# Kernel tuning notes

Hardware: AMD Instinct MI355X
Metric: run time of the kernel (lower is better)

## Reference

```python
import jax, jax.numpy as jnp
import numpy as np
from jax import lax

TOL = 1e-06
POSINF = 1000000.0
NEGINF = -1000000.0


def _grad1(x, axis):
    """torch.gradient with spacing=1, edge_order=1 along `axis`:
    central differences in the interior, one-sided at the edges."""
    n = x.shape[axis]
    left = lax.slice_in_dim(x, 0, n - 2, axis=axis)
    right = lax.slice_in_dim(x, 2, n, axis=axis)
    interior = (right - left) * 0.5
    first = lax.slice_in_dim(x, 1, 2, axis=axis) - lax.slice_in_dim(x, 0, 1, axis=axis)
    last = lax.slice_in_dim(x, n - 1, n, axis=axis) - lax.slice_in_dim(x, n - 2, n - 1, axis=axis)
    return jnp.concatenate([first, interior, last], axis=axis)


def _clean(g):
    g = jnp.nan_to_num(g, nan=0.0, posinf=POSINF, neginf=NEGINF)
    return jnp.where(jnp.abs(g) < TOL, jnp.zeros_like(g), g)


def setup_inputs() -> dict:
    key = jax.random.key(0)
    k1, k2 = jax.random.split(key)
    shape = (8, 4, 64, 128, 128)  # [B, C=4, D, H, W]
    return {
        "input": jax.random.normal(k1, shape, dtype=jnp.float32),
        "target": jax.random.normal(k2, shape, dtype=jnp.float32),
    }


def reference(input, target):
    # spacing is ones per batch, so per-batch/per-channel loops collapse into
    # one vectorized finite-difference per spatial axis (dims 2, 3, 4).
    x = input.astype(jnp.float32)
    t = target.astype(jnp.float32)
    total = jnp.float32(0.0)
    for axis in (2, 3, 4):
        diff = _clean(_grad1(x, axis)) - _clean(_grad1(t, axis))
        # per-channel MSE (mean over b,d,h,w), then summed over the 4 channels
        total = total + jnp.sum(jnp.mean(diff * diff, axis=(0, 2, 3, 4)))
    return total
```

## Files before the change

kernel.cpp:

```cpp
#include <hip/hip_runtime.h>
#include <math.h>


#define Bn 8
#define Cn 4
#define Dn 64
#define Hn 128
#define Wn 128

static constexpr int HCHUNK = 8;
static constexpr int NTHREADS = 256;
static constexpr int NBLOCKS = 4096;
static constexpr int ROW = Wn / 4;
static constexpr int PLANE = Hn * ROW;

__device__ __forceinline__ float4 sub4(const float4 a, const float4 b) {
    float4 r;
    r.x = a.x - b.x; r.y = a.y - b.y;
    r.z = a.z - b.z; r.w = a.w - b.w;
    return r;
}

__global__ __launch_bounds__(NTHREADS, 4) void gradloss_main(
        const float* __restrict__ xf, const float* __restrict__ tf,
        double* __restrict__ partials) {
    const int tid  = threadIdx.x;
    const int w4   = tid & 31;
    const int dlow = tid >> 5;
    const int b    = blockIdx.x;
    const int bc    = b & 31;
    const int hc    = (b >> 5) & 15;
    const int dhigh = b >> 9;
    const int d  = dhigh * 8 + dlow;
    const int h0 = hc * HCHUNK;

    const int base = ((bc * Dn + d) * Hn + h0) * ROW + w4;
    const float4* __restrict__ Xr = (const float4*)xf + base;
    const float4* __restrict__ Tr = (const float4*)tf + base;

    const bool haloLow  = (dlow == 0);
    const bool haloHigh = (dlow == 7);
    const bool isHalo   = haloLow | haloHigh;
    const int hoff = haloLow ? ((dhigh > 0) ? -PLANE : 0)
                             : ((dhigh < 7) ?  PLANE : 0);

    const float sd2  = (d == 0 || d == Dn - 1) ? 1.0f : 0.25f;
    const float sw02 = (w4 == 0) ? 1.0f : 0.25f;
    const float sw32 = (w4 == 31) ? 1.0f : 0.25f;

    __shared__ float4 uL[2][10][32];

    float4 uc = sub4(Xr[0], Tr[0]);
    float4 um;
    if (h0 > 0) um = sub4(Xr[-ROW], Tr[-ROW]);
    else        um = uc;
    float4 hu;
    if (isHalo) hu = sub4(Xr[hoff], Tr[hoff]);
    else        hu = make_float4(0.f, 0.f, 0.f, 0.f);

    float acc0 = 0.0f, acc1 = 0.0f, acc2 = 0.0f;
    int s = 0;
    #pragma unroll
    for (int hl = 0; hl < HCHUNK; ++hl) {
        const int h = h0 + hl;
        const int po = (h < Hn - 1) ? ROW : 0;

        const float4 xn = Xr[po], tn = Tr[po];
        float4 xh, th;
        if (isHalo) { xh = Xr[hoff + po]; th = Tr[hoff + po]; }

        uL[s][dlow + 1][w4] = uc;
        if (haloLow)  uL[s][0][w4] = hu;
        if (haloHigh) uL[s][9][w4] = hu;
        __syncthreads();

        const float4 udp = uL[s][dlow + 2][w4];
        const float4 udm = uL[s][dlow][w4];
        { const float dx = udp.x - udm.x; acc1 = fmaf(dx * dx, sd2, acc1); }
        { const float dx = udp.y - udm.y; acc1 = fmaf(dx * dx, sd2, acc1); }
        { const float dx = udp.z - udm.z; acc1 = fmaf(dx * dx, sd2, acc1); }
        { const float dx = udp.w - udm.w; acc1 = fmaf(dx * dx, sd2, acc1); }

        const float ulw = __shfl_up(uc.w, 1, 32);
        const float urx = __shfl_down(uc.x, 1, 32);
        const float ul = (w4 == 0)  ? uc.x : ulw;
        const float ur = (w4 == 31) ? uc.w : urx;
        { const float dx = uc.y - ul;   acc2 = fmaf(dx * dx, sw02, acc2); }
        { const float dx = uc.z - uc.x; acc2 = fmaf(dx * dx, 0.25f, acc2); }
        { const float dx = uc.w - uc.y; acc2 = fmaf(dx * dx, 0.25f, acc2); }
        { const float dx = ur - uc.z;   acc2 = fmaf(dx * dx, sw32, acc2); }

        const float4 un = sub4(xn, tn);
        const float sh2 = (h == 0 || h == Hn - 1) ? 1.0f : 0.25f;
        { const float dx = un.x - um.x; acc0 = fmaf(dx * dx, sh2, acc0); }
        { const float dx = un.y - um.y; acc0 = fmaf(dx * dx, sh2, acc0); }
        { const float dx = un.z - um.z; acc0 = fmaf(dx * dx, sh2, acc0); }
        { const float dx = un.w - um.w; acc0 = fmaf(dx * dx, sh2, acc0); }

        um = uc; uc = un;
        if (isHalo) hu = sub4(xh, th);
        Xr += ROW; Tr += ROW;
        s ^= 1;
    }

    float acc = (acc0 + acc1) + acc2;

    for (int off = 32; off > 0; off >>= 1)
        acc += __shfl_down(acc, off, 64);

    __shared__ float wsum[NTHREADS / 64];
    const int lane = tid & 63;
    const int wid = tid >> 6;
    if (lane == 0) wsum[wid] = acc;
    __syncthreads();
    if (tid == 0) {
        double bsum = (double)wsum[0] + (double)wsum[1] +
                      (double)wsum[2] + (double)wsum[3];
        partials[blockIdx.x] = bsum;
    }
}

__global__ __launch_bounds__(256) void gradloss_reduce(
        const double* __restrict__ partials, float* __restrict__ out, int n) {
    double a = 0.0;
    for (int i = threadIdx.x; i < n; i += 256) a += partials[i];
    for (int off = 32; off > 0; off >>= 1)
        a += __shfl_down(a, off, 64);
    __shared__ double sh[4];
    const int lane = threadIdx.x & 63;
    const int wid = threadIdx.x >> 6;
    if (lane == 0) sh[wid] = a;
    __syncthreads();
    if (threadIdx.x == 0) {
        double tot = sh[0] + sh[1] + sh[2] + sh[3];
        out[0] = (float)(tot / 8388608.0);
    }
}

extern "C" void kernel_launch(void* const* d_in, const int* in_sizes, int n_in,
                              void* d_out, int out_size, void* d_ws, size_t ws_size,
                              hipStream_t stream) {
    const float* x = (const float*)d_in[0];
    const float* t = (const float*)d_in[1];
    float* out = (float*)d_out;
    double* partials = (double*)d_ws;

    gradloss_main<<<NBLOCKS, NTHREADS, 0, stream>>>(x, t, partials);
    gradloss_reduce<<<1, 256, 0, stream>>>(partials, out, NBLOCKS);
}
```

Baseline: 284.5 us.

## Replace LDS D-neighbor exchange with direct global loads and software prefetch

Drops the shared-memory staging and per-row __syncthreads used to exchange D-neighbor planes. Each thread now loads its own D+1 and D-1 values from global memory, relying on L2/cache hits, and double-buffers the next row's loads in registers. This removes barriers and LDS traffic, but roughly triples the global load instructions per thread and raises register pressure. The occupancy hint in launch_bounds is also dropped.

```diff
diff --git a/kernel.cpp b/kernel.cpp
--- a/kernel.cpp
+++ b/kernel.cpp
@@ -21,7 +21,21 @@
     return r;
 }
 
-__global__ __launch_bounds__(NTHREADS, 4) void gradloss_main(
+struct Step {
+    float4 xp, tp;
+    float4 xdp, tdp;
+    float4 xdm, tdm;
+};
+
+__device__ __forceinline__ void issue_step(
+        const float4* __restrict__ Xr, const float4* __restrict__ Tr,
+        int po, int dpo, int dmo, Step& s) {
+    s.xp  = Xr[po];  s.tp  = Tr[po];
+    s.xdp = Xr[dpo]; s.tdp = Tr[dpo];
+    s.xdm = Xr[dmo]; s.tdm = Tr[dmo];
+}
+
+__global__ __launch_bounds__(NTHREADS) void gradloss_main(
         const float* __restrict__ xf, const float* __restrict__ tf,
         double* __restrict__ partials) {
     const int tid  = threadIdx.x;
@@ -38,48 +52,38 @@
     const float4* __restrict__ Xr = (const float4*)xf + base;
     const float4* __restrict__ Tr = (const float4*)tf + base;
 
-    const bool haloLow  = (dlow == 0);
-    const bool haloHigh = (dlow == 7);
-    const bool isHalo   = haloLow | haloHigh;
-    const int hoff = haloLow ? ((dhigh > 0) ? -PLANE : 0)
-                             : ((dhigh < 7) ?  PLANE : 0);
-
+    const int dpo = (d < Dn - 1) ? PLANE : 0;
+    const int dmo = (d > 0) ? -PLANE : 0;
     const float sd2  = (d == 0 || d == Dn - 1) ? 1.0f : 0.25f;
     const float sw02 = (w4 == 0) ? 1.0f : 0.25f;
     const float sw32 = (w4 == 31) ? 1.0f : 0.25f;
 
-    __shared__ float4 uL[2][10][32];
-
-    float4 uc = sub4(Xr[0], Tr[0]);
-    float4 um;
-    if (h0 > 0) um = sub4(Xr[-ROW], Tr[-ROW]);
-    else        um = uc;
-    float4 hu;
-    if (isHalo) hu = sub4(Xr[hoff], Tr[hoff]);
-    else        hu = make_float4(0.f, 0.f, 0.f, 0.f);
+    const int mo = (h0 > 0) ? -ROW : 0;
+    const float4 xc0 = Xr[0],  tc0 = Tr[0];
+    const float4 xm0 = Xr[mo], tm0 = Tr[mo];
+    Step sbuf[2];
+    {
+        issue_step(Xr, Tr, ROW, dpo, dmo, sbuf[0]);
+    }
+    float4 uc = sub4(xc0, tc0);
+    float4 um = sub4(xm0, tm0);
 
     float acc0 = 0.0f, acc1 = 0.0f, acc2 = 0.0f;
-    int s = 0;
     #pragma unroll
     for (int hl = 0; hl < HCHUNK; ++hl) {
         const int h = h0 + hl;
-        const int po = (h < Hn - 1) ? ROW : 0;
 
-        const float4 xn = Xr[po], tn = Tr[po];
-        float4 xh, th;
-        if (isHalo) { xh = Xr[hoff + po]; th = Tr[hoff + po]; }
+        if (hl + 1 < HCHUNK) {
+            const int po2 = (h + 1 < Hn - 1) ? ROW : 0;
+            issue_step(Xr + ROW, Tr + ROW, po2, dpo, dmo, sbuf[(hl + 1) & 1]);
+        }
 
-        uL[s][dlow + 1][w4] = uc;
-        if (haloLow)  uL[s][0][w4] = hu;
-        if (haloHigh) uL[s][9][w4] = hu;
-        __syncthreads();
+        const Step& s = sbuf[hl & 1];
 
-        const float4 udp = uL[s][dlow + 2][w4];
-        const float4 udm = uL[s][dlow][w4];
-        { const float dx = udp.x - udm.x; acc1 = fmaf(dx * dx, sd2, acc1); }
-        { const float dx = udp.y - udm.y; acc1 = fmaf(dx * dx, sd2, acc1); }
-        { const float dx = udp.z - udm.z; acc1 = fmaf(dx * dx, sd2, acc1); }
-        { const float dx = udp.w - udm.w; acc1 = fmaf(dx * dx, sd2, acc1); }
+        { const float dx = (s.xdp.x - s.xdm.x) - (s.tdp.x - s.tdm.x); acc1 = fmaf(dx * dx, sd2, acc1); }
+        { const float dx = (s.xdp.y - s.xdm.y) - (s.tdp.y - s.tdm.y); acc1 = fmaf(dx * dx, sd2, acc1); }
+        { const float dx = (s.xdp.z - s.xdm.z) - (s.tdp.z - s.tdm.z); acc1 = fmaf(dx * dx, sd2, acc1); }
+        { const float dx = (s.xdp.w - s.xdm.w) - (s.tdp.w - s.tdm.w); acc1 = fmaf(dx * dx, sd2, acc1); }
 
         const float ulw = __shfl_up(uc.w, 1, 32);
         const float urx = __shfl_down(uc.x, 1, 32);
@@ -90,7 +94,7 @@
         { const float dx = uc.w - uc.y; acc2 = fmaf(dx * dx, 0.25f, acc2); }
         { const float dx = ur - uc.z;   acc2 = fmaf(dx * dx, sw32, acc2); }
 
-        const float4 un = sub4(xn, tn);
+        const float4 un = sub4(s.xp, s.tp);
         const float sh2 = (h == 0 || h == Hn - 1) ? 1.0f : 0.25f;
         { const float dx = un.x - um.x; acc0 = fmaf(dx * dx, sh2, acc0); }
         { const float dx = un.y - um.y; acc0 = fmaf(dx * dx, sh2, acc0); }
@@ -98,9 +102,7 @@
         { const float dx = un.w - um.w; acc0 = fmaf(dx * dx, sh2, acc0); }
 
         um = uc; uc = un;
-        if (isHalo) hu = sub4(xh, th);
         Xr += ROW; Tr += ROW;
-        s ^= 1;
     }
 
     float acc = (acc0 + acc1) + acc2;
```

New measurement: 290.5 us. 2.1% more time.

## Load whole H-chunk tile up front and drop per-row block barriers

Applied to the files above, without the earlier changes.

Each thread now issues all of its row loads (10 rows of x and t plus a cooperative load of the D-halo planes) at once into registers, writes the difference field into a 3D shared tile, and syncs once. The per-row double-buffered shared exchange with a __syncthreads each iteration is removed. This raises memory-level parallelism and removes the per-row barriers and divergent halo loads. In exchange it uses more registers and shared memory, and the occupancy hint of 4 blocks per SM is dropped.

```diff
diff --git a/kernel.cpp b/kernel.cpp
--- a/kernel.cpp
+++ b/kernel.cpp
@@ -8,7 +8,6 @@
 #define Hn 128
 #define Wn 128
 
-static constexpr int HCHUNK = 8;
 static constexpr int NTHREADS = 256;
 static constexpr int NBLOCKS = 4096;
 static constexpr int ROW = Wn / 4;
@@ -21,7 +20,7 @@
     return r;
 }
 
-__global__ __launch_bounds__(NTHREADS, 4) void gradloss_main(
+__global__ __launch_bounds__(NTHREADS) void gradloss_main(
         const float* __restrict__ xf, const float* __restrict__ tf,
         double* __restrict__ partials) {
     const int tid  = threadIdx.x;
@@ -30,57 +29,76 @@
     const int b    = blockIdx.x;
     const int bc    = b & 31;
     const int hc    = (b >> 5) & 15;
-    const int dhigh = b >> 9;
-    const int d  = dhigh * 8 + dlow;
-    const int h0 = hc * HCHUNK;
+    const int dt    = b >> 9;
+    const int d  = dt * 8 + dlow;
+    const int h0 = hc * 8;
 
-    const int base = ((bc * Dn + d) * Hn + h0) * ROW + w4;
-    const float4* __restrict__ Xr = (const float4*)xf + base;
-    const float4* __restrict__ Tr = (const float4*)tf + base;
+    const float4* __restrict__ X = (const float4*)xf;
+    const float4* __restrict__ T = (const float4*)tf;
+    const int slab  = bc * (Dn * PLANE);
+    const int pbase = slab + d * PLANE;
 
-    const bool haloLow  = (dlow == 0);
-    const bool haloHigh = (dlow == 7);
-    const bool isHalo   = haloLow | haloHigh;
-    const int hoff = haloLow ? ((dhigh > 0) ? -PLANE : 0)
-                             : ((dhigh < 7) ?  PLANE : 0);
+    float4 xr[10], tr[10];
+    #pragma unroll
+    for (int r = 0; r < 10; ++r) {
+        int h = h0 + r - 1;
+        h = (h < 0) ? 0 : ((h > Hn - 1) ? Hn - 1 : h);
+        const int idx = pbase + h * ROW + w4;
+        xr[r] = X[idx];
+        tr[r] = T[idx];
+    }
+    float4 hx[2], htl[2];
+    int hwr[2];
+    #pragma unroll
+    for (int k = 0; k < 2; ++k) {
+        const int p    = tid + k * 256;
+        const int side = p >> 8;
+        const int hh   = (p >> 5) & 7;
+        const int ww   = p & 31;
+        int dh = dt * 8 + (side ? 8 : -1);
+        dh = (dh < 0) ? 0 : ((dh > Dn - 1) ? Dn - 1 : dh);
+        const int idx = slab + dh * PLANE + (h0 + hh) * ROW + ww;
+        hx[k]  = X[idx];
+        htl[k] = T[idx];
+        hwr[k] = (side ? 9 : 0) * (8 * 32) + hh * 32 + ww;
+    }
+
+    __shared__ float4 uL[10][8][32];
+    float4 u[10];
+    #pragma unroll
+    for (int r = 0; r < 10; ++r) u[r] = sub4(xr[r], tr[r]);
+    #pragma unroll
+    for (int hl = 0; hl < 8; ++hl) uL[dlow + 1][hl][w4] = u[hl + 1];
+    #pragma unroll
+    for (int k = 0; k < 2; ++k)
+        ((float4*)uL)[hwr[k]] = sub4(hx[k], htl[k]);
+    __syncthreads();
 
     const float sd2  = (d == 0 || d == Dn - 1) ? 1.0f : 0.25f;
     const float sw02 = (w4 == 0) ? 1.0f : 0.25f;
     const float sw32 = (w4 == 31) ? 1.0f : 0.25f;
 
-    __shared__ float4 uL[2][10][32];
+    float acc0 = 0.0f, acc1 = 0.0f, acc2 = 0.0f;
+    #pragma unroll
+    for (int hl = 0; hl < 8; ++hl) {
+        const int h = h0 + hl;
+        const float sh2 = (h == 0 || h == Hn - 1) ? 1.0f : 0.25f;
 
-    float4 uc = sub4(Xr[0], Tr[0]);
-    float4 um;
-    if (h0 > 0) um = sub4(Xr[-ROW], Tr[-ROW]);
-    else        um = uc;
-    float4 hu;
-    if (isHalo) hu = sub4(Xr[hoff], Tr[hoff]);
-    else        hu = make_float4(0.f, 0.f, 0.f, 0.f);
-
-    float acc0 = 0.0f, acc1 = 0.0f, acc2 = 0.0f;
-    int s = 0;
-    #pragma unroll
-    for (int hl = 0; hl < HCHUNK; ++hl) {
-        const int h = h0 + hl;
-        const int po = (h < Hn - 1) ? ROW : 0;
-
-        const float4 xn = Xr[po], tn = Tr[po];
-        float4 xh, th;
-        if (isHalo) { xh = Xr[hoff + po]; th = Tr[hoff + po]; }
-
-        uL[s][dlow + 1][w4] = uc;
-        if (haloLow)  uL[s][0][w4] = hu;
-        if (haloHigh) uL[s][9][w4] = hu;
-        __syncthreads();
-
-        const float4 udp = uL[s][dlow + 2][w4];
-        const float4 udm = uL[s][dlow][w4];
+        const float4 udp = uL[dlow + 2][hl][w4];
+        const float4 udm = uL[dlow][hl][w4];
         { const float dx = udp.x - udm.x; acc1 = fmaf(dx * dx, sd2, acc1); }
         { const float dx = udp.y - udm.y; acc1 = fmaf(dx * dx, sd2, acc1); }
         { const float dx = udp.z - udm.z; acc1 = fmaf(dx * dx, sd2, acc1); }
         { const float dx = udp.w - udm.w; acc1 = fmaf(dx * dx, sd2, acc1); }
 
+        const float4 un = u[hl + 2];
+        const float4 um = u[hl];
+        { const float dx = un.x - um.x; acc0 = fmaf(dx * dx, sh2, acc0); }
+        { const float dx = un.y - um.y; acc0 = fmaf(dx * dx, sh2, acc0); }
+        { const float dx = un.z - um.z; acc0 = fmaf(dx * dx, sh2, acc0); }
+        { const float dx = un.w - um.w; acc0 = fmaf(dx * dx, sh2, acc0); }
+
+        const float4 uc = u[hl + 1];
         const float ulw = __shfl_up(uc.w, 1, 32);
         const float urx = __shfl_down(uc.x, 1, 32);
         const float ul = (w4 == 0)  ? uc.x : ulw;
@@ -89,18 +107,6 @@
         { const float dx = uc.z - uc.x; acc2 = fmaf(dx * dx, 0.25f, acc2); }
         { const float dx = uc.w - uc.y; acc2 = fmaf(dx * dx, 0.25f, acc2); }
         { const float dx = ur - uc.z;   acc2 = fmaf(dx * dx, sw32, acc2); }
-
-        const float4 un = sub4(xn, tn);
-        const float sh2 = (h == 0 || h == Hn - 1) ? 1.0f : 0.25f;
-        { const float dx = un.x - um.x; acc0 = fmaf(dx * dx, sh2, acc0); }
-        { const float dx = un.y - um.y; acc0 = fmaf(dx * dx, sh2, acc0); }
-        { const float dx = un.z - um.z; acc0 = fmaf(dx * dx, sh2, acc0); }
-        { const float dx = un.w - um.w; acc0 = fmaf(dx * dx, sh2, acc0); }
-
-        um = uc; uc = un;
-        if (isHalo) hu = sub4(xh, th);
-        Xr += ROW; Tr += ROW;
-        s ^= 1;
     }
 
     float acc = (acc0 + acc1) + acc2;
@@ -108,7 +114,8 @@
     for (int off = 32; off > 0; off >>= 1)
         acc += __shfl_down(acc, off, 64);
 
-    __shared__ float wsum[NTHREADS / 64];
+    __syncthreads();
+    float* wsum = (float*)&uL[0][0][0];
     const int lane = tid & 63;
     const int wid = tid >> 6;
     if (lane == 0) wsum[wid] = acc;
```

Result: no change. 280.5 us (-1.4%).
